# Kernel optimization log

Measured on AMD Instinct MI355X. Metric: run time of the kernel, lower is better.

Reference implementation:

```python
import jax, jax.numpy as jnp
import numpy as np

N = 4096          # nodes
IN_F = 256        # in_features (divisible by 4)
OUT_F = 64        # out_features per head
HEADS = 4
ALPHA = 0.2       # LeakyReLU negative slope
NEG_INF = -9e15   # same masking constant as the torch code


def make_quaternion_mul(kernel):
    """kernel: [IN_F//4, OUT_F] -> hamilton: [IN_F, OUT_F].
    Mirrors the torch make_quaternion_mul (split along dim=1 into r,i,j,k)."""
    r, i, j, k = jnp.split(kernel, 4, axis=1)
    r2 = jnp.concatenate([r, -i, -j, -k], axis=1)
    i2 = jnp.concatenate([i,  r, -k,  j], axis=1)
    j2 = jnp.concatenate([j,  k,  r, -i], axis=1)
    k2 = jnp.concatenate([k, -j,  i,  r], axis=1)
    return jnp.concatenate([r2, i2, j2, k2], axis=0)


def setup_inputs() -> dict:
    key = jax.random.key(0)
    k1, k2, k3, k4 = jax.random.split(key, 4)
    x = jax.random.normal(k1, (N, IN_F), dtype=jnp.float32)
    # Glorot-ish init for quaternion kernels: [H, IN_F//4, OUT_F]
    stdv = np.sqrt(6.0 / (IN_F // 4 + OUT_F)).astype(np.float32)
    W_heads = jax.random.uniform(k2, (HEADS, IN_F // 4, OUT_F), dtype=jnp.float32,
                                 minval=-stdv, maxval=stdv)
    a_heads = jax.random.normal(k3, (HEADS, 2 * OUT_F), dtype=jnp.float32) * 0.1
    adj = (jax.random.uniform(k4, (N, N)) < 0.005).astype(jnp.float32)
    adj = jnp.maximum(adj, jnp.eye(N, dtype=jnp.float32))
    return {"x": x, "adj": adj, "W_heads": W_heads, "a_heads": a_heads}


def reference(x, adj, W_heads, a_heads):
    mask = adj > 0  # [N, N]

    def head(Wk, ak):
        hamilton = make_quaternion_mul(Wk)                # [IN_F, OUT_F]
        h = x @ hamilton                                  # [N, OUT_F]
        # e[i,j] = leakyrelu(h_i . a[:F] + h_j . a[F:]) -- equivalent to the
        # repeat/concat construction without materializing [N*N, 2F].
        e_src = h @ ak[:OUT_F]                            # [N]
        e_dst = h @ ak[OUT_F:]                            # [N]
        e = jax.nn.leaky_relu(e_src[:, None] + e_dst[None, :], negative_slope=ALPHA)
        att = jax.nn.softmax(jnp.where(mask, e, NEG_INF), axis=1)  # [N, N]
        return att @ h                                    # [N, OUT_F]

    outs = jax.vmap(head)(W_heads, a_heads)               # [H, N, OUT_F]
    out = jnp.transpose(outs, (1, 0, 2)).reshape(N, HEADS * OUT_F)
    return jax.nn.elu(out)  # concat=True path
```

## Files before the change

kernel.cpp:

```cpp
#include <hip/hip_runtime.h>

#define N 4096
#define IN_F 256
#define OUT_F 64
#define HEADS 4
#define ALPHA 0.2f
#define SEG 64

typedef __attribute__((ext_vector_type(8))) short short8;
typedef __attribute__((ext_vector_type(4))) float f32x4;

__device__ __forceinline__ unsigned short f2bf(float f) {
    unsigned u = __builtin_bit_cast(unsigned, f);
    u += 0x7fffu + ((u >> 16) & 1u);
    return (unsigned short)(u >> 16);
}

__device__ __forceinline__ float bf2f(unsigned short u) {
    return __builtin_bit_cast(float, (unsigned)u << 16);
}

__global__ __launch_bounds__(256) void k_prep(const float* __restrict__ x,
                                              const float* __restrict__ W,
                                              unsigned short* __restrict__ xb,
                                              unsigned short* __restrict__ hamT) {
    const int tid = blockIdx.x * 256 + threadIdx.x;
    const float4 xv = *reinterpret_cast<const float4*>(x + (size_t)tid * 4);
    ushort4 o;
    o.x = f2bf(xv.x); o.y = f2bf(xv.y); o.z = f2bf(xv.z); o.w = f2bf(xv.w);
    *reinterpret_cast<ushort4*>(xb + (size_t)tid * 4) = o;

    if (tid < HEADS * OUT_F * IN_F) {
        const int hd = tid >> 14, f = (tid >> 8) & 63, k = tid & 255;
        const int q = k >> 6, kr = k & 63, p = f >> 4, fr = f & 15;
        const int   comp_t[4][4] = {{0,1,2,3},{1,0,3,2},{2,3,0,1},{3,2,1,0}};
        const float sign_t[4][4] = {{1.f,-1.f,-1.f,-1.f},
                                    {1.f, 1.f,-1.f, 1.f},
                                    {1.f, 1.f, 1.f,-1.f},
                                    {1.f,-1.f, 1.f, 1.f}};
        hamT[tid] = f2bf(sign_t[q][p] * W[(hd * 64 + kr) * 64 + comp_t[q][p] * 16 + fr]);
    }
}

__global__ __launch_bounds__(256) void k_h(const unsigned short* __restrict__ xb,
                                           const unsigned short* __restrict__ hamT,
                                           const float* __restrict__ a,
                                           unsigned short* __restrict__ hb,
                                           float* __restrict__ esp,
                                           float* __restrict__ edp) {
    const int wave = threadIdx.x >> 6, lane = threadIdx.x & 63;
    const int gw = blockIdx.x * 4 + wave;
    const int rg = gw >> 3;
    const int hd = (gw >> 1) & 3;
    const int cf = gw & 1;
    const int m0 = rg * 16;
    const int r16 = lane & 15, g = lane >> 4;

    const unsigned short* xrow = xb + (size_t)(m0 + r16) * IN_F + g * 8;
    short8 af[8];
#pragma unroll
    for (int kk = 0; kk < 8; ++kk)
        af[kk] = *reinterpret_cast<const short8*>(xrow + kk * 32);

    f32x4 acc[2];
#pragma unroll
    for (int t = 0; t < 2; ++t) acc[t] = (f32x4){0.f, 0.f, 0.f, 0.f};

    const unsigned short* hbase = hamT + (size_t)(hd * 64 + cf * 32 + r16) * IN_F + g * 8;
#pragma unroll
    for (int kk = 0; kk < 8; ++kk) {
#pragma unroll
        for (int t = 0; t < 2; ++t) {
            const short8 bf = *reinterpret_cast<const short8*>(hbase + t * 16 * IN_F + kk * 32);
            acc[t] = __builtin_amdgcn_mfma_f32_16x16x32_bf16(af[kk], bf, acc[t], 0, 0, 0);
        }
    }

    float p[4] = {0.f, 0.f, 0.f, 0.f}, q[4] = {0.f, 0.f, 0.f, 0.f};
#pragma unroll
    for (int t = 0; t < 2; ++t) {
        const int fcol = cf * 32 + t * 16 + r16;
        const float as = a[hd * 128 + fcol];
        const float ad = a[hd * 128 + 64 + fcol];
#pragma unroll
        for (int j = 0; j < 4; ++j) {
            const float v = acc[t][j];
            hb[(size_t)(m0 + g * 4 + j) * (HEADS * OUT_F) + hd * 64 + fcol] = f2bf(v);
            p[j] = fmaf(v, as, p[j]);
            q[j] = fmaf(v, ad, q[j]);
        }
    }
#pragma unroll
    for (int off = 1; off < 16; off <<= 1) {
#pragma unroll
        for (int j = 0; j < 4; ++j) {
            p[j] += __shfl_xor(p[j], off);
            q[j] += __shfl_xor(q[j], off);
        }
    }
    if (r16 == 0) {
#pragma unroll
        for (int j = 0; j < 4; ++j) {
            const int row = m0 + g * 4 + j;
            esp[row * 8 + hd * 2 + cf] = p[j];
            edp[row * 8 + hd * 2 + cf] = q[j];
        }
    }
}

__global__ __launch_bounds__(256) void k_attn(const float* __restrict__ adj,
                                              const unsigned short* __restrict__ hb,
                                              const float* __restrict__ esp,
                                              const float* __restrict__ edp,
                                              float* __restrict__ out) {
    __shared__ int   s_seg[4][SEG];
    __shared__ int   s_cnt[4];
    __shared__ int   s_all[4 * SEG];
    __shared__ float s_z[4][4 * SEG];

    const int wave = threadIdx.x >> 6;
    const int lane = threadIdx.x & 63;
    const int i = blockIdx.x;

    const uint4* arow = reinterpret_cast<const uint4*>(adj + (size_t)i * N) + wave * 256;
    uint4 av[4];
#pragma unroll
    for (int c = 0; c < 4; ++c) av[c] = arow[c * 64 + lane];

    const unsigned long long lmask_lt = (lane == 63) ? ~0ull >> 1
                                                     : (1ull << lane) - 1ull;
    int base = 0;
#pragma unroll
    for (int c = 0; c < 4; ++c) {
#pragma unroll
        for (int s = 0; s < 4; ++s) {
            const unsigned v = (s == 0) ? av[c].x : (s == 1) ? av[c].y
                             : (s == 2) ? av[c].z : av[c].w;
            const bool hit = v != 0u;
            const unsigned long long mk = __ballot(hit);
            if (hit) {
                const int pos = base + __popcll(mk & lmask_lt);
                if (pos < SEG)
                    s_seg[wave][pos] = wave * 1024 + c * 256 + lane * 4 + s;
            }
            base += __popcll(mk);
        }
    }
    if (lane == 0) s_cnt[wave] = base < SEG ? base : SEG;
    __syncthreads();

    const int c0 = s_cnt[0], c1 = s_cnt[1], c2 = s_cnt[2], c3 = s_cnt[3];
    const int wbase = (wave > 0 ? c0 : 0) + (wave > 1 ? c1 : 0) + (wave > 2 ? c2 : 0);
    const int wcnt = s_cnt[wave];
    if (lane < wcnt) s_all[wbase + lane] = s_seg[wave][lane];
    __syncthreads();
    const int cnt = c0 + c1 + c2 + c3;

    const int hd = wave;
    const float es = esp[i * 8 + hd * 2] + esp[i * 8 + hd * 2 + 1];
    float mh = -3.0e38f;
    for (int e = lane; e < cnt; e += 64) {
        const int j = s_all[e];
        const float ed = edp[j * 8 + hd * 2] + edp[j * 8 + hd * 2 + 1];
        float z = es + ed;
        z = z > 0.f ? z : ALPHA * z;
        s_z[hd][e] = z;
        mh = fmaxf(mh, z);
    }
#pragma unroll
    for (int off = 32; off > 0; off >>= 1) mh = fmaxf(mh, __shfl_xor(mh, off));

    float lsum = 0.f, acc = 0.f;
    int e = 0;
    for (; e + 4 <= cnt; e += 4) {
        const int j0 = s_all[e], j1 = s_all[e + 1], j2 = s_all[e + 2], j3 = s_all[e + 3];
        const unsigned short u0 = hb[(size_t)j0 * 256 + threadIdx.x];
        const unsigned short u1 = hb[(size_t)j1 * 256 + threadIdx.x];
        const unsigned short u2 = hb[(size_t)j2 * 256 + threadIdx.x];
        const unsigned short u3 = hb[(size_t)j3 * 256 + threadIdx.x];
        const float w0 = __expf(s_z[hd][e]     - mh);
        const float w1 = __expf(s_z[hd][e + 1] - mh);
        const float w2 = __expf(s_z[hd][e + 2] - mh);
        const float w3 = __expf(s_z[hd][e + 3] - mh);
        lsum += w0 + w1 + w2 + w3;
        acc = fmaf(w0, bf2f(u0), acc);
        acc = fmaf(w1, bf2f(u1), acc);
        acc = fmaf(w2, bf2f(u2), acc);
        acc = fmaf(w3, bf2f(u3), acc);
    }
    for (; e < cnt; ++e) {
        const int j = s_all[e];
        const unsigned short u = hb[(size_t)j * 256 + threadIdx.x];
        const float w = __expf(s_z[hd][e] - mh);
        lsum += w;
        acc = fmaf(w, bf2f(u), acc);
    }

    const float v = acc / lsum;
    out[(size_t)i * 256 + threadIdx.x] = v > 0.f ? v : __expf(v) - 1.f;
}

extern "C" void kernel_launch(void* const* d_in, const int* in_sizes, int n_in,
                              void* d_out, int out_size, void* d_ws, size_t ws_size,
                              hipStream_t stream) {
    const float* x   = (const float*)d_in[0];
    const float* adj = (const float*)d_in[1];
    const float* W   = (const float*)d_in[2];
    const float* a   = (const float*)d_in[3];
    float* out = (float*)d_out;

    float* ws   = (float*)d_ws;
    float* esp  = ws;
    float* edp  = esp + N * 8;
    unsigned short* hb   = (unsigned short*)(edp + N * 8);
    unsigned short* xb   = hb + (size_t)N * 256;
    unsigned short* hamT = xb + (size_t)N * IN_F;

    k_prep<<<1024, 256, 0, stream>>>(x, W, xb, hamT);
    k_h<<<512, 256, 0, stream>>>(xb, hamT, a, hb, esp, edp);
    k_attn<<<N, 256, 0, stream>>>(adj, hb, esp, edp, out);
}
```

Before: 39.50 us.

## Fuse bf16 conversion and quaternion weight expansion into the projection kernel

Removes the separate prep kernel that converted x to bf16 and built the transposed Hamilton matrix, and instead converts x and builds the weight fragments on the fly inside the projection kernel. Each wave now computes one 16-column slice (four slices per head), which doubles the grid and writes four partial attention logits per head that the attention kernel sums with a float4 load. This saves a kernel launch and the intermediate bf16 round trip through global memory. In exchange it re-reads fp32 x once per column slice and does strided scalar loads of W.

```diff
diff --git a/kernel.cpp b/kernel.cpp
--- a/kernel.cpp
+++ b/kernel.cpp
@@ -20,90 +20,84 @@
     return __builtin_bit_cast(float, (unsigned)u << 16);
 }
 
-__global__ __launch_bounds__(256) void k_prep(const float* __restrict__ x,
+__global__ __launch_bounds__(256, 4) void k_h(const float* __restrict__ x,
                                               const float* __restrict__ W,
-                                              unsigned short* __restrict__ xb,
-                                              unsigned short* __restrict__ hamT) {
-    const int tid = blockIdx.x * 256 + threadIdx.x;
-    const float4 xv = *reinterpret_cast<const float4*>(x + (size_t)tid * 4);
-    ushort4 o;
-    o.x = f2bf(xv.x); o.y = f2bf(xv.y); o.z = f2bf(xv.z); o.w = f2bf(xv.w);
-    *reinterpret_cast<ushort4*>(xb + (size_t)tid * 4) = o;
-
-    if (tid < HEADS * OUT_F * IN_F) {
-        const int hd = tid >> 14, f = (tid >> 8) & 63, k = tid & 255;
-        const int q = k >> 6, kr = k & 63, p = f >> 4, fr = f & 15;
-        const int   comp_t[4][4] = {{0,1,2,3},{1,0,3,2},{2,3,0,1},{3,2,1,0}};
-        const float sign_t[4][4] = {{1.f,-1.f,-1.f,-1.f},
-                                    {1.f, 1.f,-1.f, 1.f},
-                                    {1.f, 1.f, 1.f,-1.f},
-                                    {1.f,-1.f, 1.f, 1.f}};
-        hamT[tid] = f2bf(sign_t[q][p] * W[(hd * 64 + kr) * 64 + comp_t[q][p] * 16 + fr]);
-    }
-}
-
-__global__ __launch_bounds__(256) void k_h(const unsigned short* __restrict__ xb,
-                                           const unsigned short* __restrict__ hamT,
-                                           const float* __restrict__ a,
-                                           unsigned short* __restrict__ hb,
-                                           float* __restrict__ esp,
-                                           float* __restrict__ edp) {
+                                              const float* __restrict__ a,
+                                              unsigned short* __restrict__ hb,
+                                              float* __restrict__ esp,
+                                              float* __restrict__ edp) {
     const int wave = threadIdx.x >> 6, lane = threadIdx.x & 63;
     const int gw = blockIdx.x * 4 + wave;
-    const int rg = gw >> 3;
-    const int hd = (gw >> 1) & 3;
-    const int cf = gw & 1;
+    const int rg = gw >> 4;
+    const int hd = (gw >> 2) & 3;
+    const int cq = gw & 3;
     const int m0 = rg * 16;
     const int r16 = lane & 15, g = lane >> 4;
 
-    const unsigned short* xrow = xb + (size_t)(m0 + r16) * IN_F + g * 8;
+    const int   comp_t[4][4] = {{0,1,2,3},{1,0,3,2},{2,3,0,1},{3,2,1,0}};
+    const float sign_t[4][4] = {{1.f,-1.f,-1.f,-1.f},
+                                {1.f, 1.f,-1.f, 1.f},
+                                {1.f, 1.f, 1.f,-1.f},
+                                {1.f,-1.f, 1.f, 1.f}};
+
+    const float* xrow = x + (size_t)(m0 + r16) * IN_F + g * 8;
     short8 af[8];
 #pragma unroll
+    for (int kk = 0; kk < 8; ++kk) {
+        const float4 u0 = *reinterpret_cast<const float4*>(xrow + kk * 32);
+        const float4 u1 = *reinterpret_cast<const float4*>(xrow + kk * 32 + 4);
+        short8 t;
+        t[0] = (short)f2bf(u0.x); t[1] = (short)f2bf(u0.y);
+        t[2] = (short)f2bf(u0.z); t[3] = (short)f2bf(u0.w);
+        t[4] = (short)f2bf(u1.x); t[5] = (short)f2bf(u1.y);
+        t[6] = (short)f2bf(u1.z); t[7] = (short)f2bf(u1.w);
+        af[kk] = t;
+    }
+
+    short8 bfr[8];
+#pragma unroll
+    for (int kk = 0; kk < 8; ++kk) {
+        const int q = kk >> 1;
+        const int kr0 = (kk & 1) * 32 + g * 8;
+        const float s = sign_t[q][cq];
+        const int c = comp_t[q][cq];
+        const float* wp = W + (size_t)(hd * 64 + kr0) * 64 + c * 16 + r16;
+        short8 t;
+#pragma unroll
+        for (int j = 0; j < 8; ++j) t[j] = (short)f2bf(s * wp[j * 64]);
+        bfr[kk] = t;
+    }
+
+    f32x4 acc = (f32x4){0.f, 0.f, 0.f, 0.f};
+#pragma unroll
     for (int kk = 0; kk < 8; ++kk)
-        af[kk] = *reinterpret_cast<const short8*>(xrow + kk * 32);
-
-    f32x4 acc[2];
-#pragma unroll
-    for (int t = 0; t < 2; ++t) acc[t] = (f32x4){0.f, 0.f, 0.f, 0.f};
-
-    const unsigned short* hbase = hamT + (size_t)(hd * 64 + cf * 32 + r16) * IN_F + g * 8;
-#pragma unroll
-    for (int kk = 0; kk < 8; ++kk) {
-#pragma unroll
-        for (int t = 0; t < 2; ++t) {
-            const short8 bf = *reinterpret_cast<const short8*>(hbase + t * 16 * IN_F + kk * 32);
-            acc[t] = __builtin_amdgcn_mfma_f32_16x16x32_bf16(af[kk], bf, acc[t], 0, 0, 0);
-        }
-    }
-
-    float p[4] = {0.f, 0.f, 0.f, 0.f}, q[4] = {0.f, 0.f, 0.f, 0.f};
-#pragma unroll
-    for (int t = 0; t < 2; ++t) {
-        const int fcol = cf * 32 + t * 16 + r16;
-        const float as = a[hd * 128 + fcol];
-        const float ad = a[hd * 128 + 64 + fcol];
-#pragma unroll
-        for (int j = 0; j < 4; ++j) {
-            const float v = acc[t][j];
-            hb[(size_t)(m0 + g * 4 + j) * (HEADS * OUT_F) + hd * 64 + fcol] = f2bf(v);
-            p[j] = fmaf(v, as, p[j]);
-            q[j] = fmaf(v, ad, q[j]);
-        }
+        acc = __builtin_amdgcn_mfma_f32_16x16x32_bf16(af[kk], bfr[kk], acc, 0, 0, 0);
+
+    const int f = cq * 16 + r16;
+    const float as = a[hd * 128 + f];
+    const float ad = a[hd * 128 + 64 + f];
+    float p[4], q2[4];
+#pragma unroll
+    for (int j = 0; j < 4; ++j) {
+        const float v = acc[j];
+        hb[(size_t)(m0 + g * 4 + j) * (HEADS * OUT_F) + hd * 64 + f] = f2bf(v);
+        p[j] = v * as;
+        q2[j] = v * ad;
     }
 #pragma unroll
     for (int off = 1; off < 16; off <<= 1) {
 #pragma unroll
         for (int j = 0; j < 4; ++j) {
             p[j] += __shfl_xor(p[j], off);
-            q[j] += __shfl_xor(q[j], off);
+            q2[j] += __shfl_xor(q2[j], off);
         }
     }
     if (r16 == 0) {
 #pragma unroll
         for (int j = 0; j < 4; ++j) {
             const int row = m0 + g * 4 + j;
-            esp[row * 8 + hd * 2 + cf] = p[j];
-            edp[row * 8 + hd * 2 + cf] = q[j];
+            esp[row * 16 + hd * 4 + cq] = p[j];
+            edp[row * 16 + hd * 4 + cq] = q2[j];
         }
     }
 }
@@ -157,11 +151,13 @@
     const int cnt = c0 + c1 + c2 + c3;
 
     const int hd = wave;
-    const float es = esp[i * 8 + hd * 2] + esp[i * 8 + hd * 2 + 1];
+    const float4 es4 = *reinterpret_cast<const float4*>(&esp[i * 16 + hd * 4]);
+    const float es = (es4.x + es4.y) + (es4.z + es4.w);
     float mh = -3.0e38f;
     for (int e = lane; e < cnt; e += 64) {
         const int j = s_all[e];
-        const float ed = edp[j * 8 + hd * 2] + edp[j * 8 + hd * 2 + 1];
+        const float4 ed4 = *reinterpret_cast<const float4*>(&edp[j * 16 + hd * 4]);
+        const float ed = (ed4.x + ed4.y) + (ed4.z + ed4.w);
         float z = es + ed;
         z = z > 0.f ? z : ALPHA * z;
         s_z[hd][e] = z;
@@ -209,14 +205,11 @@
     const float* a   = (const float*)d_in[3];
     float* out = (float*)d_out;
 
-    float* ws   = (float*)d_ws;
-    float* esp  = ws;
-    float* edp  = esp + N * 8;
-    unsigned short* hb   = (unsigned short*)(edp + N * 8);
-    unsigned short* xb   = hb + (size_t)N * 256;
-    unsigned short* hamT = xb + (size_t)N * IN_F;
-
-    k_prep<<<1024, 256, 0, stream>>>(x, W, xb, hamT);
-    k_h<<<512, 256, 0, stream>>>(xb, hamT, a, hb, esp, edp);
+    float* ws  = (float*)d_ws;
+    float* esp = ws;
+    float* edp = esp + N * 16;
+    unsigned short* hb = (unsigned short*)(edp + N * 16);
+
+    k_h<<<1024, 256, 0, stream>>>(x, W, a, hb, esp, edp);
     k_attn<<<N, 256, 0, stream>>>(adj, hb, esp, edp, out);
 }
```

After: 39.02 us. About the same (-1.2%).
